# Optimization experiments

Hardware: AMD Instinct MI355X
Metric: run time of the kernel (lower is better)

## Reference

```python
import jax, jax.numpy as jnp
import numpy as np

N_QUBITS = 10
N_LAYERS = 4
BATCH = 16384


def setup_inputs() -> dict:
    key = jax.random.key(0)
    k1, k2 = jax.random.split(key)
    x = jax.random.normal(k1, (BATCH, N_LAYERS * N_QUBITS), dtype=jnp.float32)
    weight = jax.random.normal(k2, (N_LAYERS, N_QUBITS, 2), dtype=jnp.float32) * 0.1
    return {"x": x, "weight": weight}


def _apply_1q(state, U, q):
    # state: [B, 2, 2, ..., 2] (axis 1+q is wire q); U: [B, 2, 2] batched unitary
    s = jnp.moveaxis(state, 1 + q, -1)
    s = jnp.einsum('bij,b...j->b...i', U, s)
    return jnp.moveaxis(s, -1, 1 + q)


def _apply_cnot(state, c, t):
    # CNOT with control wire c, target wire t: flip target where control==1
    s = jnp.moveaxis(state, (1 + c, 1 + t), (-2, -1))
    s = jnp.stack([s[..., 0, :], s[..., 1, ::-1]], axis=-2)
    return jnp.moveaxis(s, (-2, -1), (1 + c, 1 + t))


def _ry(theta):
    # theta: [...]; returns [..., 2, 2] real rotation matrix RY(theta)
    c, s = jnp.cos(theta * 0.5), jnp.sin(theta * 0.5)
    return jnp.stack([jnp.stack([c, -s], -1), jnp.stack([s, c], -1)], -2)


def _forward(x, weight):
    B = x.shape[0]
    # data re-uploading angles: atan(x) * pi, shape [B, L, Q]
    a = jnp.arctan(x.reshape(B, N_LAYERS, N_QUBITS)) * jnp.pi
    Rin = _ry(a).astype(jnp.complex64)                       # [B,L,Q,2,2]
    w0, w1 = weight[..., 0], weight[..., 1]                  # [L,Q]
    # RZ(w0) = diag(e^{-i w0/2}, e^{+i w0/2}); composing scales rows of RY
    phase = jnp.stack([jnp.exp(-0.5j * w0), jnp.exp(0.5j * w0)], -1)  # [L,Q,2]
    Rw = _ry(w1).astype(jnp.complex64)                       # [L,Q,2,2]
    M = Rin * phase[None, :, :, :, None]                     # RZ(w0) @ RY(a)
    U = jnp.einsum('lqij,blqjk->blqik', Rw, M)               # RY(w1)@RZ(w0)@RY(a)

    # |0...0> state, shape [B] + [2]*N_QUBITS
    state = jnp.zeros((B,) + (2,) * N_QUBITS, jnp.complex64)
    state = state.at[(slice(None),) + (0,) * N_QUBITS].set(1.0)

    for l in range(N_LAYERS):
        for q in range(N_QUBITS):
            state = _apply_1q(state, U[:, l, q], q)
        for q in range(N_QUBITS):
            state = _apply_cnot(state, q, (q + 1) % N_QUBITS)

    probs = state.real ** 2 + state.imag ** 2
    outs = []
    for q in range(N_QUBITS):
        p = jnp.moveaxis(probs, 1 + q, 1).reshape(B, 2, -1).sum(-1)
        outs.append(p[:, 0] - p[:, 1])  # <Z_q> = P(0) - P(1)
    return jnp.stack(outs, -1).astype(jnp.float32)


def reference(x, weight):
    return _forward(x, weight)
```

## Files before the change

### kernel.cpp

```cpp
#include <hip/hip_runtime.h>
#include <hip/hip_fp16.h>
#include <math.h>

#define NQ 10
#define NL 4
#define NA (NQ * NL)
#define PI_F 3.14159265358979323846f

typedef _Float16 h2 __attribute__((ext_vector_type(2)));

template <int SR, int SI>
__device__ __forceinline__ unsigned cmul_sg(unsigned c, unsigned s) {
  unsigned d;
  if constexpr (SR > 0) {
    asm("v_pk_mul_f16 %0, %1, %2 op_sel_hi:[0,1]" : "=v"(d) : "v"(c), "v"(s));
  } else {
    asm("v_pk_mul_f16 %0, %1, %2 op_sel_hi:[0,1] neg_lo:[1,0] neg_hi:[1,0]"
        : "=v"(d) : "v"(c), "v"(s));
  }
  if constexpr (SI > 0) {
    asm("v_pk_fma_f16 %0, %1, %2, %0 op_sel:[1,1,0] op_sel_hi:[1,0,1] neg_lo:[1,0,0]"
        : "+v"(d) : "v"(c), "v"(s));
  } else {
    asm("v_pk_fma_f16 %0, %1, %2, %0 op_sel:[1,1,0] op_sel_hi:[1,0,1] neg_hi:[1,0,0]"
        : "+v"(d) : "v"(c), "v"(s));
  }
  return d;
}

template <int SR, int SI>
__device__ __forceinline__ unsigned cfma_sg(unsigned c, unsigned s, unsigned acc) {
  unsigned d;
  if constexpr (SR > 0) {
    asm("v_pk_fma_f16 %0, %1, %2, %3 op_sel_hi:[0,1,1]"
        : "=v"(d) : "v"(c), "v"(s), "v"(acc));
  } else {
    asm("v_pk_fma_f16 %0, %1, %2, %3 op_sel_hi:[0,1,1] neg_lo:[1,0,0] neg_hi:[1,0,0]"
        : "=v"(d) : "v"(c), "v"(s), "v"(acc));
  }
  if constexpr (SI > 0) {
    asm("v_pk_fma_f16 %0, %1, %2, %0 op_sel:[1,1,0] op_sel_hi:[1,0,1] neg_lo:[1,0,0]"
        : "+v"(d) : "v"(c), "v"(s));
  } else {
    asm("v_pk_fma_f16 %0, %1, %2, %0 op_sel:[1,1,0] op_sel_hi:[1,0,1] neg_hi:[1,0,0]"
        : "+v"(d) : "v"(c), "v"(s));
  }
  return d;
}

template <int MASK>
__device__ __forceinline__ int ishfl_xor(int v) {
  if constexpr (MASK == 1) {
    return __builtin_amdgcn_update_dpp(v, v, 0xB1, 0xF, 0xF, true);
  } else if constexpr (MASK == 2) {
    return __builtin_amdgcn_update_dpp(v, v, 0x4E, 0xF, 0xF, true);
  } else if constexpr (MASK == 4) {
    return __builtin_amdgcn_ds_swizzle(v, 0x101F);
  } else if constexpr (MASK == 8) {
    return __builtin_amdgcn_update_dpp(v, v, 0x128, 0xF, 0xF, true);
  } else if constexpr (MASK == 16) {
    return __builtin_amdgcn_ds_swizzle(v, 0x401F);
  } else {
    return __shfl_xor(v, MASK, 64);
  }
}

template <int MASK>
__device__ __forceinline__ float fshfl_xor(float v) {
  return __int_as_float(ishfl_xor<MASK>(__float_as_int(v)));
}

__device__ __forceinline__ unsigned readlane_u(unsigned v, int l) {
  return (unsigned)__builtin_amdgcn_readlane((int)v, l);
}

__device__ __forceinline__ float wave_sum_h(float v) {
  v += fshfl_xor<1>(v);
  v += fshfl_xor<2>(v);
  v += fshfl_xor<4>(v);
  v += fshfl_xor<8>(v);
  v += fshfl_xor<16>(v);
  v += fshfl_xor<32>(v);
  return v;
}

__device__ __forceinline__ unsigned pack_h2_rtn(float re, float im) {
  return (unsigned)__half_as_ushort(__float2half(re)) |
         ((unsigned)__half_as_ushort(__float2half(im)) << 16);
}

template <int LB>
__device__ __forceinline__ void cross_gate2(unsigned (&sv)[2][16],
                                            const unsigned (&u00)[2],
                                            const unsigned (&u01)[2], int lane) {
  const bool bit = (lane & (1 << LB)) != 0;
  unsigned A[2], B[2];
#pragma unroll
  for (int e = 0; e < 2; ++e) {
    A[e] = bit ? (u00[e] ^ 0x80000000u) : u00[e];
    B[e] = bit ? (u01[e] ^ 0x00008000u) : u01[e];
  }
#pragma unroll
  for (int r = 0; r < 16; ++r) {
    unsigned p0 = (unsigned)ishfl_xor<(1 << LB)>((int)sv[0][r]);
    unsigned p1 = (unsigned)ishfl_xor<(1 << LB)>((int)sv[1][r]);
    sv[0][r] = cfma_sg<1, 1>(B[0], p0, cmul_sg<1, 1>(A[0], sv[0][r]));
    sv[1][r] = cfma_sg<1, 1>(B[1], p1, cmul_sg<1, 1>(A[1], sv[1][r]));
  }
}

template <int LB>
__device__ __forceinline__ void cross_gate2_r0(unsigned (&sv)[2][16],
                                               const unsigned (&u00)[2],
                                               const unsigned (&u01)[2], int lane) {
  const bool bit = (lane & (1 << LB)) != 0;
#pragma unroll
  for (int e = 0; e < 2; ++e) {
    const unsigned A = bit ? (u00[e] ^ 0x80000000u) : u00[e];
    const unsigned B = bit ? (u01[e] ^ 0x00008000u) : u01[e];
    unsigned p = (unsigned)ishfl_xor<(1 << LB)>((int)sv[e][0]);
    sv[e][0] = cfma_sg<1, 1>(B, p, cmul_sg<1, 1>(A, sv[e][0]));
  }
}

template <int RB>
__device__ __forceinline__ void local_gate2(unsigned (&sv)[2][16],
                                            const unsigned (&u00)[2],
                                            const unsigned (&u01)[2]) {
#pragma unroll
  for (int rlo = 0; rlo < 16; ++rlo) {
    if (rlo & (1 << RB)) continue;
    const int rhi = rlo | (1 << RB);
#pragma unroll
    for (int e = 0; e < 2; ++e) {
      unsigned lo = sv[e][rlo], hi = sv[e][rhi];
      sv[e][rlo] = cfma_sg<1, 1>(u01[e], hi, cmul_sg<1, 1>(u00[e], lo));
      sv[e][rhi] = cfma_sg<1, -1>(u00[e], hi, cmul_sg<-1, 1>(u01[e], lo));
    }
  }
}

template <int RB>
__device__ __forceinline__ void local_gate2_fill(unsigned (&sv)[2][16],
                                                 const unsigned (&u00)[2],
                                                 const unsigned (&u01)[2]) {
#pragma unroll
  for (int rlo = 0; rlo < 16; ++rlo) {
    if (rlo & ((2 << RB) - 1)) continue;
    const int rhi = rlo | (1 << RB);
#pragma unroll
    for (int e = 0; e < 2; ++e) {
      unsigned lo = sv[e][rlo];
      sv[e][rhi] = cmul_sg<-1, 1>(u01[e], lo);
      sv[e][rlo] = cmul_sg<1, 1>(u00[e], lo);
    }
  }
}

__device__ __forceinline__ void ring_step(unsigned (&sv)[2][16], int lane,
                                          int permSrc) {
#pragma unroll
  for (int r = 0; r < 16; ++r) {
    sv[0][r] = (unsigned)__shfl((int)sv[0][r], permSrc);
    sv[1][r] = (unsigned)__shfl((int)sv[1][r], permSrc);
  }
  {
    const bool c5 = (lane & 1) != 0;
#pragma unroll
    for (int r = 0; r < 8; ++r) {
#pragma unroll
      for (int e = 0; e < 2; ++e) {
        unsigned a = sv[e][r], b = sv[e][r + 8];
        sv[e][r] = c5 ? b : a;
        sv[e][r + 8] = c5 ? a : b;
      }
    }
  }
#pragma unroll
  for (int e = 0; e < 2; ++e) {
    unsigned t;
    t = sv[e][2]; sv[e][2] = sv[e][3]; sv[e][3] = t;
    t = sv[e][4]; sv[e][4] = sv[e][6]; sv[e][6] = sv[e][5]; sv[e][5] = sv[e][7]; sv[e][7] = t;
    t = sv[e][8]; sv[e][8] = sv[e][12]; sv[e][12] = sv[e][10]; sv[e][10] = sv[e][15]; sv[e][15] = t;
    t = sv[e][9]; sv[e][9] = sv[e][13]; sv[e][13] = sv[e][11]; sv[e][11] = sv[e][14]; sv[e][14] = t;
  }
#pragma unroll
  for (int r = 1; r < 16; r += 2) {
    sv[0][r] = (unsigned)ishfl_xor<32>((int)sv[0][r]);
    sv[1][r] = (unsigned)ishfl_xor<32>((int)sv[1][r]);
  }
}

__global__ __launch_bounds__(256, 4) void qsim_kernel(
    const float* __restrict__ x, const float* __restrict__ w,
    float* __restrict__ out, int batch) {
  const int lane = threadIdx.x & 63;
  const int wv = blockIdx.x * 4 + (threadIdx.x >> 6);
  const int permSrc = lane ^ (lane >> 1);

  float Pr = 0.f, Pi = 0.f, Qr = 0.f, Qi = 0.f;
  if (lane < NA) {
    float w0 = w[2 * lane], w1 = w[2 * lane + 1];
    float sphi, cphi, sw, cw;
    sincosf(0.5f * w0, &sphi, &cphi);
    sincosf(0.5f * w1, &sw, &cw);
    Pr = cw * cphi; Pi = -cw * sphi;
    Qr = sw * cphi; Qi = sw * sphi;
  }

  unsigned U00[2] = {0u, 0u}, U01[2] = {0u, 0u};
#pragma unroll
  for (int e = 0; e < 2; ++e) {
    const int wid = wv * 2 + e;
    const int widc = wid < batch ? wid : batch - 1;
    if (lane < NA) {
      float xv = x[widc * NA + lane];
      float a = 0.5f * PI_F * atanf(xv);
      float sa, ca;
      sincosf(a, &sa, &ca);
      float u00r = ca * Pr - sa * Qr;
      float u00i = ca * Pi - sa * Qi;
      float u01r = -(sa * Pr + ca * Qr);
      float u01i = -(sa * Pi + ca * Qi);
      U00[e] = pack_h2_rtn(u00r, u00i);
      U01[e] = pack_h2_rtn(u01r, u01i);
    }
  }

  unsigned sv[2][16];
#pragma unroll
  for (int r = 0; r < 16; ++r) { sv[0][r] = 0u; sv[1][r] = 0u; }
  if (lane == 0) { sv[0][0] = 0x3C00u; sv[1][0] = 0x3C00u; }

#define GET_U(j)                                                     \
  const unsigned u00[2] = {readlane_u(U00[0], (j)), readlane_u(U00[1], (j))}; \
  const unsigned u01[2] = {readlane_u(U01[0], (j)), readlane_u(U01[1], (j))}

  { GET_U(0); cross_gate2_r0<5>(sv, u00, u01, lane); }
  { GET_U(1); cross_gate2_r0<4>(sv, u00, u01, lane); }
  { GET_U(2); cross_gate2_r0<3>(sv, u00, u01, lane); }
  { GET_U(3); cross_gate2_r0<2>(sv, u00, u01, lane); }
  { GET_U(4); cross_gate2_r0<1>(sv, u00, u01, lane); }
  { GET_U(5); cross_gate2_r0<0>(sv, u00, u01, lane); }
  { GET_U(6); local_gate2_fill<3>(sv, u00, u01); }
  { GET_U(7); local_gate2_fill<2>(sv, u00, u01); }
  { GET_U(8); local_gate2_fill<1>(sv, u00, u01); }
  { GET_U(9); local_gate2_fill<0>(sv, u00, u01); }
  ring_step(sv, lane, permSrc);

#pragma unroll 1
  for (int l = 1; l < NL; ++l) {
    const int j0 = l * NQ;
    { GET_U(j0 + 0); cross_gate2<5>(sv, u00, u01, lane); }
    { GET_U(j0 + 1); cross_gate2<4>(sv, u00, u01, lane); }
    { GET_U(j0 + 2); cross_gate2<3>(sv, u00, u01, lane); }
    { GET_U(j0 + 3); cross_gate2<2>(sv, u00, u01, lane); }
    { GET_U(j0 + 4); cross_gate2<1>(sv, u00, u01, lane); }
    { GET_U(j0 + 5); cross_gate2<0>(sv, u00, u01, lane); }
    { GET_U(j0 + 6); local_gate2<3>(sv, u00, u01); }
    { GET_U(j0 + 7); local_gate2<2>(sv, u00, u01); }
    { GET_U(j0 + 8); local_gate2<1>(sv, u00, u01); }
    { GET_U(j0 + 9); local_gate2<0>(sv, u00, u01); }
    ring_step(sv, lane, permSrc);
  }
#undef GET_U

#pragma unroll
  for (int e = 0; e < 2; ++e) {
    const int wid = wv * 2 + e;
    float tot = 0.f, t0 = 0.f, t1 = 0.f, t2 = 0.f, t3 = 0.f;
#pragma unroll
    for (int r = 0; r < 16; ++r) {
      h2 a = __builtin_bit_cast(h2, sv[e][r]);
      float re = (float)a.x, im = (float)a.y;
      float pv = re * re + im * im;
      tot += pv;
      if (r & 1) t0 += pv;
      if (r & 2) t1 += pv;
      if (r & 4) t2 += pv;
      if (r & 8) t3 += pv;
    }
    const float S3 = wave_sum_h(t3);
    const float S2 = wave_sum_h(t2);
    const float S1 = wave_sum_h(t1);
    const float S0 = wave_sum_h(t0);
    const float N = wave_sum_h(tot);
    const float invN = 1.0f / N;
    float v = tot, h;
    h = fshfl_xor<1>(v);  v = (lane & 1)  ? h - v : v + h;
    h = fshfl_xor<2>(v);  v = (lane & 2)  ? h - v : v + h;
    h = fshfl_xor<4>(v);  v = (lane & 4)  ? h - v : v + h;
    h = fshfl_xor<8>(v);  v = (lane & 8)  ? h - v : v + h;
    h = fshfl_xor<16>(v); v = (lane & 16) ? h - v : v + h;
    h = fshfl_xor<32>(v); v = (lane & 32) ? h - v : v + h;

    if (wid < batch) {
      float* o = out + wid * NQ;
      if (lane == 32) o[0] = v * invN;
      if (lane == 16) o[1] = v * invN;
      if (lane == 8)  o[2] = v * invN;
      if (lane == 4)  o[3] = v * invN;
      if (lane == 2)  o[4] = v * invN;
      if (lane == 1)  o[5] = v * invN;
      if (lane == 0) {
        o[6] = (v - 2.f * S3) * invN;
        o[7] = (v - 2.f * S2) * invN;
        o[8] = (v - 2.f * S1) * invN;
        o[9] = (v - 2.f * S0) * invN;
      }
    }
  }
}

extern "C" void kernel_launch(void* const* d_in, const int* in_sizes, int n_in,
                              void* d_out, int out_size, void* d_ws, size_t ws_size,
                              hipStream_t stream) {
  const float* x = (const float*)d_in[0];
  const float* w = (const float*)d_in[1];
  float* out = (float*)d_out;
  const int batch = in_sizes[0] / NA;
  const int waves = (batch + 1) / 2;
  const int blocks = (waves + 3) / 4;
  qsim_kernel<<<blocks, 256, 0, stream>>>(x, w, out, batch);
}
```

Before: 134.5 us.

## Mix DPP and ds_swizzle shuffles, use hardware sin/cos and fdot2

For the second interleaved batch element, the xor-shuffles for masks 1, 2 and 8 now use ds_swizzle instead of DPP. The intent is to split shuffle traffic between the VALU/DPP path and the LDS crossbar so the two streams can overlap. The setup trig is replaced with hardware sin/cos intrinsics on revolution-scaled angles, which gives up the accuracy and range reduction of sincosf. The final probability sums use fdot2 on the packed fp16 amplitudes, cutting the conversions and multiplies.

New measurement: 132.5 us. About the same (-1.5%).

```diff
diff --git a/kernel.cpp b/kernel.cpp
--- a/kernel.cpp
+++ b/kernel.cpp
@@ -6,6 +6,7 @@
 #define NL 4
 #define NA (NQ * NL)
 #define PI_F 3.14159265358979323846f
+#define INV_2PI_F 0.15915494309189535f
 
 typedef _Float16 h2 __attribute__((ext_vector_type(2)));
 
@@ -65,6 +66,23 @@
   }
 }
 
+template <int MASK, int E>
+__device__ __forceinline__ int ishfl_xor_e(int v) {
+  if constexpr (E == 1) {
+    if constexpr (MASK == 1) {
+      return __builtin_amdgcn_ds_swizzle(v, 0x041F);
+    } else if constexpr (MASK == 2) {
+      return __builtin_amdgcn_ds_swizzle(v, 0x081F);
+    } else if constexpr (MASK == 8) {
+      return __builtin_amdgcn_ds_swizzle(v, 0x201F);
+    } else {
+      return ishfl_xor<MASK>(v);
+    }
+  } else {
+    return ishfl_xor<MASK>(v);
+  }
+}
+
 template <int MASK>
 __device__ __forceinline__ float fshfl_xor(float v) {
   return __int_as_float(ishfl_xor<MASK>(__float_as_int(v)));
@@ -102,8 +120,8 @@
   }
 #pragma unroll
   for (int r = 0; r < 16; ++r) {
-    unsigned p0 = (unsigned)ishfl_xor<(1 << LB)>((int)sv[0][r]);
-    unsigned p1 = (unsigned)ishfl_xor<(1 << LB)>((int)sv[1][r]);
+    unsigned p0 = (unsigned)ishfl_xor_e<(1 << LB), 0>((int)sv[0][r]);
+    unsigned p1 = (unsigned)ishfl_xor_e<(1 << LB), 1>((int)sv[1][r]);
     sv[0][r] = cfma_sg<1, 1>(B[0], p0, cmul_sg<1, 1>(A[0], sv[0][r]));
     sv[1][r] = cfma_sg<1, 1>(B[1], p1, cmul_sg<1, 1>(A[1], sv[1][r]));
   }
@@ -114,12 +132,17 @@
                                                const unsigned (&u00)[2],
                                                const unsigned (&u01)[2], int lane) {
   const bool bit = (lane & (1 << LB)) != 0;
-#pragma unroll
-  for (int e = 0; e < 2; ++e) {
-    const unsigned A = bit ? (u00[e] ^ 0x80000000u) : u00[e];
-    const unsigned B = bit ? (u01[e] ^ 0x00008000u) : u01[e];
-    unsigned p = (unsigned)ishfl_xor<(1 << LB)>((int)sv[e][0]);
-    sv[e][0] = cfma_sg<1, 1>(B, p, cmul_sg<1, 1>(A, sv[e][0]));
+  {
+    const unsigned A = bit ? (u00[0] ^ 0x80000000u) : u00[0];
+    const unsigned B = bit ? (u01[0] ^ 0x00008000u) : u01[0];
+    unsigned p = (unsigned)ishfl_xor_e<(1 << LB), 0>((int)sv[0][0]);
+    sv[0][0] = cfma_sg<1, 1>(B, p, cmul_sg<1, 1>(A, sv[0][0]));
+  }
+  {
+    const unsigned A = bit ? (u00[1] ^ 0x80000000u) : u00[1];
+    const unsigned B = bit ? (u01[1] ^ 0x00008000u) : u01[1];
+    unsigned p = (unsigned)ishfl_xor_e<(1 << LB), 1>((int)sv[1][0]);
+    sv[1][0] = cfma_sg<1, 1>(B, p, cmul_sg<1, 1>(A, sv[1][0]));
   }
 }
 
@@ -201,9 +224,9 @@
   float Pr = 0.f, Pi = 0.f, Qr = 0.f, Qi = 0.f;
   if (lane < NA) {
     float w0 = w[2 * lane], w1 = w[2 * lane + 1];
-    float sphi, cphi, sw, cw;
-    sincosf(0.5f * w0, &sphi, &cphi);
-    sincosf(0.5f * w1, &sw, &cw);
+    float r0 = w0 * (0.5f * INV_2PI_F), r1 = w1 * (0.5f * INV_2PI_F);
+    float sphi = __builtin_amdgcn_sinf(r0), cphi = __builtin_amdgcn_cosf(r0);
+    float sw = __builtin_amdgcn_sinf(r1), cw = __builtin_amdgcn_cosf(r1);
     Pr = cw * cphi; Pi = -cw * sphi;
     Qr = sw * cphi; Qi = sw * sphi;
   }
@@ -215,9 +238,9 @@
     const int widc = wid < batch ? wid : batch - 1;
     if (lane < NA) {
       float xv = x[widc * NA + lane];
-      float a = 0.5f * PI_F * atanf(xv);
-      float sa, ca;
-      sincosf(a, &sa, &ca);
+      float rev = 0.25f * atanf(xv);
+      float sa = __builtin_amdgcn_sinf(rev);
+      float ca = __builtin_amdgcn_cosf(rev);
       float u00r = ca * Pr - sa * Qr;
       float u00i = ca * Pi - sa * Qi;
       float u01r = -(sa * Pr + ca * Qr);
@@ -272,13 +295,11 @@
 #pragma unroll
     for (int r = 0; r < 16; ++r) {
       h2 a = __builtin_bit_cast(h2, sv[e][r]);
-      float re = (float)a.x, im = (float)a.y;
-      float pv = re * re + im * im;
-      tot += pv;
-      if (r & 1) t0 += pv;
-      if (r & 2) t1 += pv;
-      if (r & 4) t2 += pv;
-      if (r & 8) t3 += pv;
+      tot = __builtin_amdgcn_fdot2(a, a, tot, false);
+      if (r & 1) t0 = __builtin_amdgcn_fdot2(a, a, t0, false);
+      if (r & 2) t1 = __builtin_amdgcn_fdot2(a, a, t1, false);
+      if (r & 4) t2 = __builtin_amdgcn_fdot2(a, a, t2, false);
+      if (r & 8) t3 = __builtin_amdgcn_fdot2(a, a, t3, false);
     }
     const float S3 = wave_sum_h(t3);
     const float S2 = wave_sum_h(t2);
```

## Defer qubit-9 swap to the next layer, use native trig, DPP, and fdot2

Applied to the files above, without the earlier changes.

Replaces the xor-4 ds_swizzle with two DPP row ops, and uses hardware sin/cos in revolutions instead of the libm sincosf. It also folds the ring step's lane-32 exchange into the next layer's first cross gate by swapping operand roles on odd registers, and computes probabilities with fdot2. The launch bounds are removed as well. These are several separate micro-optimisations that cut shuffle and ALU work. They risk lower trig accuracy and a change in register allocation.

Measured after the change: 135.8 us. No clear change (+1.0%).

```diff
diff --git a/kernel.cpp b/kernel.cpp
--- a/kernel.cpp
+++ b/kernel.cpp
@@ -6,6 +6,7 @@
 #define NL 4
 #define NA (NQ * NL)
 #define PI_F 3.14159265358979323846f
+#define INV_2PI_F 0.15915494309189535f
 
 typedef _Float16 h2 __attribute__((ext_vector_type(2)));
 
@@ -55,7 +56,8 @@
   } else if constexpr (MASK == 2) {
     return __builtin_amdgcn_update_dpp(v, v, 0x4E, 0xF, 0xF, true);
   } else if constexpr (MASK == 4) {
-    return __builtin_amdgcn_ds_swizzle(v, 0x101F);
+    int t = __builtin_amdgcn_update_dpp(v, v, 0x141, 0xF, 0xF, true);
+    return __builtin_amdgcn_update_dpp(t, t, 0x1B, 0xF, 0xF, true);
   } else if constexpr (MASK == 8) {
     return __builtin_amdgcn_update_dpp(v, v, 0x128, 0xF, 0xF, true);
   } else if constexpr (MASK == 16) {
@@ -89,7 +91,7 @@
          ((unsigned)__half_as_ushort(__float2half(im)) << 16);
 }
 
-template <int LB>
+template <int LB, bool DEF = false>
 __device__ __forceinline__ void cross_gate2(unsigned (&sv)[2][16],
                                             const unsigned (&u00)[2],
                                             const unsigned (&u01)[2], int lane) {
@@ -104,8 +106,13 @@
   for (int r = 0; r < 16; ++r) {
     unsigned p0 = (unsigned)ishfl_xor<(1 << LB)>((int)sv[0][r]);
     unsigned p1 = (unsigned)ishfl_xor<(1 << LB)>((int)sv[1][r]);
-    sv[0][r] = cfma_sg<1, 1>(B[0], p0, cmul_sg<1, 1>(A[0], sv[0][r]));
-    sv[1][r] = cfma_sg<1, 1>(B[1], p1, cmul_sg<1, 1>(A[1], sv[1][r]));
+    if (DEF && (r & 1)) {
+      sv[0][r] = cfma_sg<1, 1>(B[0], sv[0][r], cmul_sg<1, 1>(A[0], p0));
+      sv[1][r] = cfma_sg<1, 1>(B[1], sv[1][r], cmul_sg<1, 1>(A[1], p1));
+    } else {
+      sv[0][r] = cfma_sg<1, 1>(B[0], p0, cmul_sg<1, 1>(A[0], sv[0][r]));
+      sv[1][r] = cfma_sg<1, 1>(B[1], p1, cmul_sg<1, 1>(A[1], sv[1][r]));
+    }
   }
 }
 
@@ -158,7 +165,7 @@
 }
 
 __device__ __forceinline__ void ring_step(unsigned (&sv)[2][16], int lane,
-                                          int permSrc) {
+                                          int permSrc, bool apply_q9) {
 #pragma unroll
   for (int r = 0; r < 16; ++r) {
     sv[0][r] = (unsigned)__shfl((int)sv[0][r], permSrc);
@@ -184,14 +191,16 @@
     t = sv[e][8]; sv[e][8] = sv[e][12]; sv[e][12] = sv[e][10]; sv[e][10] = sv[e][15]; sv[e][15] = t;
     t = sv[e][9]; sv[e][9] = sv[e][13]; sv[e][13] = sv[e][11]; sv[e][11] = sv[e][14]; sv[e][14] = t;
   }
-#pragma unroll
-  for (int r = 1; r < 16; r += 2) {
-    sv[0][r] = (unsigned)ishfl_xor<32>((int)sv[0][r]);
-    sv[1][r] = (unsigned)ishfl_xor<32>((int)sv[1][r]);
-  }
-}
-
-__global__ __launch_bounds__(256, 4) void qsim_kernel(
+  if (apply_q9) {
+#pragma unroll
+    for (int r = 1; r < 16; r += 2) {
+      sv[0][r] = (unsigned)ishfl_xor<32>((int)sv[0][r]);
+      sv[1][r] = (unsigned)ishfl_xor<32>((int)sv[1][r]);
+    }
+  }
+}
+
+__global__ void qsim_kernel(
     const float* __restrict__ x, const float* __restrict__ w,
     float* __restrict__ out, int batch) {
   const int lane = threadIdx.x & 63;
@@ -201,9 +210,9 @@
   float Pr = 0.f, Pi = 0.f, Qr = 0.f, Qi = 0.f;
   if (lane < NA) {
     float w0 = w[2 * lane], w1 = w[2 * lane + 1];
-    float sphi, cphi, sw, cw;
-    sincosf(0.5f * w0, &sphi, &cphi);
-    sincosf(0.5f * w1, &sw, &cw);
+    float r0 = w0 * (0.5f * INV_2PI_F), r1 = w1 * (0.5f * INV_2PI_F);
+    float sphi = __builtin_amdgcn_sinf(r0), cphi = __builtin_amdgcn_cosf(r0);
+    float sw = __builtin_amdgcn_sinf(r1), cw = __builtin_amdgcn_cosf(r1);
     Pr = cw * cphi; Pi = -cw * sphi;
     Qr = sw * cphi; Qi = sw * sphi;
   }
@@ -215,9 +224,9 @@
     const int widc = wid < batch ? wid : batch - 1;
     if (lane < NA) {
       float xv = x[widc * NA + lane];
-      float a = 0.5f * PI_F * atanf(xv);
-      float sa, ca;
-      sincosf(a, &sa, &ca);
+      float rev = 0.25f * atanf(xv);
+      float sa = __builtin_amdgcn_sinf(rev);
+      float ca = __builtin_amdgcn_cosf(rev);
       float u00r = ca * Pr - sa * Qr;
       float u00i = ca * Pi - sa * Qi;
       float u01r = -(sa * Pr + ca * Qr);
@@ -246,12 +255,12 @@
   { GET_U(7); local_gate2_fill<2>(sv, u00, u01); }
   { GET_U(8); local_gate2_fill<1>(sv, u00, u01); }
   { GET_U(9); local_gate2_fill<0>(sv, u00, u01); }
-  ring_step(sv, lane, permSrc);
+  ring_step(sv, lane, permSrc, false);
 
 #pragma unroll 1
   for (int l = 1; l < NL; ++l) {
     const int j0 = l * NQ;
-    { GET_U(j0 + 0); cross_gate2<5>(sv, u00, u01, lane); }
+    { GET_U(j0 + 0); cross_gate2<5, true>(sv, u00, u01, lane); }
     { GET_U(j0 + 1); cross_gate2<4>(sv, u00, u01, lane); }
     { GET_U(j0 + 2); cross_gate2<3>(sv, u00, u01, lane); }
     { GET_U(j0 + 3); cross_gate2<2>(sv, u00, u01, lane); }
@@ -261,7 +270,7 @@
     { GET_U(j0 + 7); local_gate2<2>(sv, u00, u01); }
     { GET_U(j0 + 8); local_gate2<1>(sv, u00, u01); }
     { GET_U(j0 + 9); local_gate2<0>(sv, u00, u01); }
-    ring_step(sv, lane, permSrc);
+    ring_step(sv, lane, permSrc, (l == NL - 1));
   }
 #undef GET_U
 
@@ -272,13 +281,11 @@
 #pragma unroll
     for (int r = 0; r < 16; ++r) {
       h2 a = __builtin_bit_cast(h2, sv[e][r]);
-      float re = (float)a.x, im = (float)a.y;
-      float pv = re * re + im * im;
-      tot += pv;
-      if (r & 1) t0 += pv;
-      if (r & 2) t1 += pv;
-      if (r & 4) t2 += pv;
-      if (r & 8) t3 += pv;
+      tot = __builtin_amdgcn_fdot2(a, a, tot, false);
+      if (r & 1) t0 = __builtin_amdgcn_fdot2(a, a, t0, false);
+      if (r & 2) t1 = __builtin_amdgcn_fdot2(a, a, t1, false);
+      if (r & 4) t2 = __builtin_amdgcn_fdot2(a, a, t2, false);
+      if (r & 8) t3 = __builtin_amdgcn_fdot2(a, a, t3, false);
     }
     const float S3 = wave_sum_h(t3);
     const float S2 = wave_sum_h(t2);
```
